# Optimization experiments

Hardware: AMD Instinct MI355X
Metric: run time of the kernel (lower is better)

## Reference

```python
import jax, jax.numpy as jnp
import numpy as np

SIG_DEPTH = 4  # matches sig_depth init arg


def _outer(a, b):
    # flattened tensor product: [B, m] x [B, n] -> [B, m*n] (row-major, matches signatory layout)
    return (a[:, :, None] * b[:, None, :]).reshape(a.shape[0], -1)


def setup_inputs() -> dict:
    key = jax.random.key(0)
    k1, k2 = jax.random.split(key)
    B, L, Cin = 64, 256, 7
    out_dim = 512
    C = Cin + 1
    sig_channels = sum(C ** k for k in range(1, SIG_DEPTH + 1))  # 4680
    inp = jax.random.normal(k1, (B, L, Cin), dtype=jnp.float32)
    W = jax.random.normal(k2, (out_dim, sig_channels), dtype=jnp.float32) * 0.02
    b = jnp.zeros((out_dim,), dtype=jnp.float32)
    return {"inp": inp, "W": W, "b": b}


def reference(inp, W, b):
    B, L, Cin = inp.shape
    # Augment: prepend time channel linspace(0, 1, L), keep original channels
    t = jnp.broadcast_to(jnp.linspace(0.0, 1.0, L, dtype=inp.dtype)[None, :, None], (B, L, 1))
    x = jnp.concatenate([t, inp], axis=-1)  # [B, L, C]
    C = Cin + 1
    d = SIG_DEPTH
    dx = jnp.transpose(x[:, 1:] - x[:, :-1], (1, 0, 2))  # [L-1, B, C] increments
    init = tuple(jnp.zeros((B, C ** (k + 1)), x.dtype) for k in range(d))  # identity signature (all zero levels)

    def step(levels, v):
        # exp(v) in the truncated tensor algebra: e_k = v^{(x)k} / k!
        e = [v]
        for k in range(1, d):
            e.append(_outer(e[-1], v) / (k + 1))
        # Chen's identity: new_k = a_k + e_k + sum_{i=1}^{k-1} a_i (x) e_{k-i}
        new = []
        for k in range(d):
            acc = levels[k] + e[k]
            for i in range(k):
                acc = acc + _outer(levels[i], e[k - 1 - i])
            new.append(acc)
        sig = jnp.concatenate(new, axis=-1)  # [B, sig_channels]
        return tuple(new), sig

    _, sigs = jax.lax.scan(step, init, dx)  # [L-1, B, sig_channels] (stream=True)
    sigs = jnp.transpose(sigs, (1, 0, 2))   # [B, L-1, sig_channels]
    return sigs @ W.T + b                   # [B, L-1, out_dim]
```

## Files before the change

### kernel.cpp

```cpp
#include <hip/hip_runtime.h>
#include <hip/hip_bf16.h>

#define BATCH 64
#define LSEQ 256
#define CIN 7
#define CC 8
#define NSIG 4680
#define KPAD 4736
#define TSTEPS 255
#define ODIM 512
#define NCHUNK 16
#define CH 16
#define NKT 74
#define BM 256
#define BN 128
#define WCVT_BLK 592

typedef __attribute__((ext_vector_type(8))) unsigned short ushort8;
typedef __attribute__((ext_vector_type(8))) __bf16 bf16x8;
typedef __attribute__((ext_vector_type(4))) float f32x4;

__device__ __forceinline__ unsigned short f2bf(float x) {
    __hip_bfloat16 h = __float2bfloat16(x);
    return *(unsigned short*)&h;
}

#define GLDS16(gp, lp)                                                      \
    __builtin_amdgcn_global_load_lds(                                       \
        (const __attribute__((address_space(1))) void*)(gp),                \
        (__attribute__((address_space(3))) void*)(lp), 16, 0, 0)

__global__ __launch_bounds__(512) void prep_kernel(const float* __restrict__ inp,
                                                   float* __restrict__ ckpt,
                                                   const float* __restrict__ W,
                                                   unsigned short* __restrict__ Wb,
                                                   int nb) {
    __shared__ float sDx[TSTEPS * CC];
    const int bx  = blockIdx.x;
    const int tid = threadIdx.x;

    if (bx < 4 * nb) {
        const int b = bx >> 2, q = bx & 3;
        const float* ip = inp + (size_t)b * LSEQ * CIN;
        for (int i = tid; i < TSTEPS * CC; i += 512) {
            int t = i >> 3, c = i & 7;
            sDx[i] = (c == 0) ? (1.0f / 255.0f)
                              : ip[(t + 1) * CIN + (c - 1)] - ip[t * CIN + (c - 1)];
        }
        __syncthreads();

        const int o  = q * 128 + (tid >> 2);
        const int e2 = tid & 3;
        const int i1 = o >> 6, i2 = (o >> 3) & 7, i3 = o & 7;
        float a1 = 0.0f, a2 = 0.0f, a3 = 0.0f, a4a = 0.0f, a4b = 0.0f;

        for (int t = 0; t < 240; ++t) {
            const float* v = &sDx[t * CC];
            const float va = v[i1], vb = v[i2], vc = v[i3];
            const float vA = v[e2], vB = v[e2 + 4];
            const float e3s = va * vb * vc * (1.0f / 6.0f);
            const float T4 = e3s * 0.25f + a1 * vb * vc * (1.0f / 6.0f)
                           + a2 * vc * 0.5f + a3;
            a4a += vA * T4;
            a4b += vB * T4;
            a3 += e3s + (a1 * vb * 0.5f + a2) * vc;
            a2 += vb * (0.5f * va + a1);
            a1 += va;

            if (((t + 1) & 15) == 0) {
                const int c = ((t + 1) >> 4) - 1;
                float* cp = ckpt + ((size_t)b * 15 + c) * NSIG;
                cp[584 + o * 8 + e2]     = a4a;
                cp[584 + o * 8 + e2 + 4] = a4b;
                if (e2 == 0) {
                    cp[72 + o] = a3;
                    if ((o & 7) == 0)  cp[8 + (o >> 3)] = a2;
                    if ((o & 63) == 0) cp[i1] = a1;
                }
            }
        }
    } else {
        const int vid = (bx - 4 * nb) * 512 + tid;
        if (vid < ODIM * (KPAD / 8)) {
            const int n = vid / (KPAD / 8);
            const int g = vid - n * (KPAD / 8);
            ushort8 pk;
            if (g < NSIG / 8) {
                const float* wp = W + (size_t)n * NSIG + g * 8;
                float4 f0 = *(const float4*)wp;
                float4 f1 = *(const float4*)(wp + 4);
                pk[0] = f2bf(f0.x); pk[1] = f2bf(f0.y);
                pk[2] = f2bf(f0.z); pk[3] = f2bf(f0.w);
                pk[4] = f2bf(f1.x); pk[5] = f2bf(f1.y);
                pk[6] = f2bf(f1.z); pk[7] = f2bf(f1.w);
            } else {
#pragma unroll
                for (int e = 0; e < 8; ++e) pk[e] = 0;
            }
            *(ushort8*)(Wb + (size_t)n * KPAD + g * 8) = pk;
        }
    }
}

__global__ __launch_bounds__(512) void sig_write_kernel(const float* __restrict__ inp,
                                                        const float* __restrict__ ckpt,
                                                        unsigned short* __restrict__ sig) {
    __shared__ float sDx[CH * CC];

    const int chunk = blockIdx.x;
    const int b     = blockIdx.y;
    const int tid   = threadIdx.x;
    const int t0    = chunk * CH;
    const int t1    = (chunk == NCHUNK - 1) ? TSTEPS : t0 + CH;

    const float* ip = inp + (size_t)b * LSEQ * CIN;
    for (int i = tid; i < (t1 - t0) * CC; i += 512) {
        int t = t0 + (i >> 3), c = i & 7;
        sDx[i] = (c == 0) ? (1.0f / 255.0f)
                          : ip[(t + 1) * CIN + (c - 1)] - ip[t * CIN + (c - 1)];
    }
    __syncthreads();

    const int i1 = tid >> 6;
    const int i2 = (tid >> 3) & 7;
    const int i3 = tid & 7;

    float a1own, a2own, a3;
    float a4[8];
    if (chunk == 0) {
        a1own = a2own = a3 = 0.0f;
#pragma unroll
        for (int e = 0; e < 8; ++e) a4[e] = 0.0f;
    } else {
        const float* cp = ckpt + ((size_t)b * 15 + (chunk - 1)) * NSIG;
        a1own = cp[i1];
        a2own = cp[8 + (tid >> 3)];
        a3    = cp[72 + tid];
        float4 q0 = *(const float4*)&cp[584 + tid * 8];
        float4 q1 = *(const float4*)&cp[584 + tid * 8 + 4];
        a4[0] = q0.x; a4[1] = q0.y; a4[2] = q0.z; a4[3] = q0.w;
        a4[4] = q1.x; a4[5] = q1.y; a4[6] = q1.z; a4[7] = q1.w;
    }

    for (int t = t0; t < t1; ++t) {
        const float* v = &sDx[(t - t0) * CC];
        const float4 vlo = *(const float4*)&v[0];
        const float4 vhi = *(const float4*)&v[4];
        const float va = v[i1], vb = v[i2], vc = v[i3];
        const float e3s = va * vb * vc * (1.0f / 6.0f);
        const float T4 = e3s * 0.25f + a1own * vb * vc * (1.0f / 6.0f)
                       + a2own * vc * 0.5f + a3;
        a4[0] += vlo.x * T4; a4[1] += vlo.y * T4;
        a4[2] += vlo.z * T4; a4[3] += vlo.w * T4;
        a4[4] += vhi.x * T4; a4[5] += vhi.y * T4;
        a4[6] += vhi.z * T4; a4[7] += vhi.w * T4;
        a3 += e3s + (a1own * vb * 0.5f + a2own) * vc;
        a2own += vb * (0.5f * va + a1own);
        a1own += va;

        unsigned short* row = sig + ((size_t)b * TSTEPS + t) * KPAD;
        ushort8 pack;
#pragma unroll
        for (int e = 0; e < 8; ++e) pack[e] = f2bf(a4[e]);
        *(ushort8*)(row + 584 + tid * 8) = pack;
        row[72 + tid] = f2bf(a3);
        if ((tid & 63) == 0) row[i1] = f2bf(a1own);
        if ((tid & 7) == 0) row[8 + (tid >> 3)] = f2bf(a2own);
        if (tid >= 448 && tid < 504) row[4232 + tid] = 0;
    }
}

__global__ __launch_bounds__(512) void gemm_kernel(const unsigned short* __restrict__ A,
                                                   const unsigned short* __restrict__ Wb,
                                                   const float* __restrict__ bias,
                                                   float* __restrict__ out,
                                                   int Mrows) {
    __shared__ unsigned short As[3][BM * 64];
    __shared__ unsigned short Bs[3][BN * 64];

    const int tid = threadIdx.x;
    int nt, mt;
    if (gridDim.y == 64) {
        const int li = blockIdx.y * 4 + blockIdx.x;
        const int x  = li & 7;
        const int j  = li >> 3;
        mt = x * 8 + (j >> 2);
        nt = j & 3;
    } else {
        nt = blockIdx.x; mt = blockIdx.y;
    }
    const int lane = tid & 63;
    const int wv   = tid >> 6;
    const int wr   = wv >> 1;
    const int wc   = wv & 1;
    const int lr   = lane & 15;
    const int lq   = lane >> 4;
    const int sb   = lr & 7;

    const f32x4 z4 = {0.0f, 0.0f, 0.0f, 0.0f};
    f32x4 acc[4][4];
#pragma unroll
    for (int i = 0; i < 4; ++i)
#pragma unroll
        for (int j = 0; j < 4; ++j) acc[i][j] = z4;

    const int srow = tid >> 3;
    const int gcb  = (tid & 7) ^ (srow & 7);
    const int scol = gcb * 8;

    const unsigned short* aptr[4];
    const unsigned short* bptr[2];
#pragma unroll
    for (int i = 0; i < 4; ++i) {
        int gr = mt * BM + i * 64 + srow;
        if (gr >= Mrows) gr = 0;
        aptr[i] = A + (size_t)gr * KPAD + scol;
    }
#pragma unroll
    for (int i = 0; i < 2; ++i)
        bptr[i] = Wb + (size_t)(nt * BN + i * 64 + srow) * KPAD + scol;

    const int kel0 = ((lq)     ^ sb) * 8;
    const int kel1 = ((4 + lq) ^ sb) * 8;
    const int aoff = (wr * 64 + lr) * 64;
    const int boff = (wc * 64 + lr) * 64;

#define STAGE_ALL(BUF, koff)                                                \
    do {                                                                    \
        _Pragma("unroll")                                                   \
        for (int i_ = 0; i_ < 4; ++i_)                                      \
            GLDS16(aptr[i_] + (koff),                                       \
                   ((char*)As[BUF]) + i_ * 8192 + tid * 16);                \
        _Pragma("unroll")                                                   \
        for (int i_ = 0; i_ < 2; ++i_)                                      \
            GLDS16(bptr[i_] + (koff),                                       \
                   ((char*)Bs[BUF]) + i_ * 8192 + tid * 16);                \
    } while (0)

#define MFMA16(AF, BF)                                                      \
    do {                                                                    \
        _Pragma("unroll")                                                   \
        for (int im_ = 0; im_ < 4; ++im_)                                   \
            _Pragma("unroll")                                               \
            for (int jm_ = 0; jm_ < 4; ++jm_)                               \
                acc[im_][jm_] = __builtin_amdgcn_mfma_f32_16x16x32_bf16(    \
                    AF[im_], BF[jm_], acc[im_][jm_], 0, 0, 0);              \
    } while (0)

#define LDF(DST, SRC, BASE, KEL)                                            \
    do {                                                                    \
        _Pragma("unroll")                                                   \
        for (int l_ = 0; l_ < 4; ++l_)                                      \
            DST[l_] = *(const bf16x8*)&SRC[(BASE) + l_ * 1024 + (KEL)];     \
    } while (0)

    bf16x8 afP[4], bfP[4], afN[4], bfN[4];

    STAGE_ALL(0, 0);
    STAGE_ALL(1, 64);
    asm volatile("s_waitcnt vmcnt(6)" ::: "memory");
    __builtin_amdgcn_sched_barrier(0);
    __builtin_amdgcn_s_barrier();
    __builtin_amdgcn_sched_barrier(0);
    LDF(afP, (&As[0][0]), aoff, kel0);
    LDF(bfP, (&Bs[0][0]), boff, kel0);
    __builtin_amdgcn_sched_barrier(0);

    int koff = 128;

#define TILE_FULL(CUR, NXT, NN)                                             \
    {                                                                       \
        LDF(afN, (&As[CUR][0]), aoff, kel1);                                \
        LDF(bfN, (&Bs[CUR][0]), boff, kel1);                                \
        STAGE_ALL(NN, koff);                                                \
        koff += 64;                                                         \
        __builtin_amdgcn_sched_barrier(0);                                  \
        asm volatile("s_waitcnt lgkmcnt(8)" ::: "memory");                  \
        __builtin_amdgcn_sched_barrier(0);                                  \
        __builtin_amdgcn_s_setprio(1);                                      \
        MFMA16(afP, bfP);                                                   \
        __builtin_amdgcn_s_setprio(0);                                      \
        __builtin_amdgcn_sched_barrier(0);                                  \
        asm volatile("s_waitcnt lgkmcnt(0)" ::: "memory");                  \
        __builtin_amdgcn_sched_barrier(0);                                  \
        asm volatile("s_waitcnt vmcnt(6)" ::: "memory");                    \
        __builtin_amdgcn_sched_barrier(0);                                  \
        __builtin_amdgcn_s_barrier();                                       \
        __builtin_amdgcn_sched_barrier(0);                                  \
        LDF(afP, (&As[NXT][0]), aoff, kel0);                                \
        LDF(bfP, (&Bs[NXT][0]), boff, kel0);                                \
        __builtin_amdgcn_sched_barrier(0);                                  \
        __builtin_amdgcn_s_setprio(1);                                      \
        MFMA16(afN, bfN);                                                   \
        __builtin_amdgcn_s_setprio(0);                                      \
        __builtin_amdgcn_sched_barrier(0);                                  \
    }

    for (int tb = 0; tb < 24; ++tb) {
        TILE_FULL(0, 1, 2);
        TILE_FULL(1, 2, 0);
        TILE_FULL(2, 0, 1);
    }

    {
        LDF(afN, (&As[0][0]), aoff, kel1);
        LDF(bfN, (&Bs[0][0]), boff, kel1);
        __builtin_amdgcn_sched_barrier(0);
        asm volatile("s_waitcnt lgkmcnt(8)" ::: "memory");
        __builtin_amdgcn_sched_barrier(0);
        __builtin_amdgcn_s_setprio(1);
        MFMA16(afP, bfP);
        __builtin_amdgcn_s_setprio(0);
        __builtin_amdgcn_sched_barrier(0);
        asm volatile("s_waitcnt lgkmcnt(0)" ::: "memory");
        __builtin_amdgcn_sched_barrier(0);
        asm volatile("s_waitcnt vmcnt(0)" ::: "memory");
        __builtin_amdgcn_sched_barrier(0);
        __builtin_amdgcn_s_barrier();
        __builtin_amdgcn_sched_barrier(0);
        LDF(afP, (&As[1][0]), aoff, kel0);
        LDF(bfP, (&Bs[1][0]), boff, kel0);
        __builtin_amdgcn_sched_barrier(0);
        __builtin_amdgcn_s_setprio(1);
        MFMA16(afN, bfN);
        __builtin_amdgcn_s_setprio(0);
        __builtin_amdgcn_sched_barrier(0);
    }
    {
        LDF(afN, (&As[1][0]), aoff, kel1);
        LDF(bfN, (&Bs[1][0]), boff, kel1);
        __builtin_amdgcn_sched_barrier(0);
        asm volatile("s_waitcnt lgkmcnt(8)" ::: "memory");
        __builtin_amdgcn_sched_barrier(0);
        __builtin_amdgcn_s_setprio(1);
        MFMA16(afP, bfP);
        __builtin_amdgcn_s_setprio(0);
        __builtin_amdgcn_sched_barrier(0);
        asm volatile("s_waitcnt lgkmcnt(0)" ::: "memory");
        __builtin_amdgcn_sched_barrier(0);
        __builtin_amdgcn_s_setprio(1);
        MFMA16(afN, bfN);
        __builtin_amdgcn_s_setprio(0);
        __builtin_amdgcn_sched_barrier(0);
    }

    float bn[4];
#pragma unroll
    for (int j = 0; j < 4; ++j)
        bn[j] = bias[nt * BN + wc * 64 + j * 16 + lr];

#pragma unroll
    for (int i = 0; i < 4; ++i) {
        const int mbase = mt * BM + wr * 64 + i * 16 + lq * 4;
#pragma unroll
        for (int r = 0; r < 4; ++r) {
            const int m = mbase + r;
            if (m < Mrows) {
#pragma unroll
                for (int j = 0; j < 4; ++j) {
                    const int n = nt * BN + wc * 64 + j * 16 + lr;
                    out[(size_t)m * ODIM + n] = acc[i][j][r] + bn[j];
                }
            }
        }
    }
#undef STAGE_ALL
#undef MFMA16
#undef LDF
#undef TILE_FULL
}

extern "C" void kernel_launch(void* const* d_in, const int* in_sizes, int n_in,
                              void* d_out, int out_size, void* d_ws, size_t ws_size,
                              hipStream_t stream) {
    const float* inp  = (const float*)d_in[0];
    const float* W    = (const float*)d_in[1];
    const float* bias = (const float*)d_in[2];
    float* out = (float*)d_out;

    const size_t wbBytes = (size_t)ODIM * KPAD * sizeof(unsigned short);
    const size_t sigPB   = (size_t)TSTEPS * KPAD * sizeof(unsigned short);
    const size_t ckptPB  = (size_t)15 * NSIG * sizeof(float);
    const size_t perB    = sigPB + ckptPB;

    int nbMax = (int)((ws_size - wbBytes) / perB);
    if (nbMax > BATCH) nbMax = BATCH;
    if (nbMax < 1) nbMax = 1;

    unsigned short* sig  = (unsigned short*)d_ws;
    float*          ckpt = (float*)((char*)d_ws + (size_t)nbMax * sigPB);
    unsigned short* Wb   = (unsigned short*)((char*)d_ws + (ws_size - wbBytes));

    for (int b0 = 0; b0 < BATCH; b0 += nbMax) {
        const int nb = (b0 + nbMax <= BATCH) ? nbMax : (BATCH - b0);
        const int Mrows = nb * TSTEPS;
        const float* ipb = inp + (size_t)b0 * LSEQ * CIN;
        prep_kernel<<<4 * nb + WCVT_BLK, 512, 0, stream>>>(ipb, ckpt, W, Wb, nb);
        sig_write_kernel<<<dim3(NCHUNK, nb), 512, 0, stream>>>(ipb, ckpt, sig);
        gemm_kernel<<<dim3(ODIM / BN, (Mrows + BM - 1) / BM), 512, 0, stream>>>(
            sig, Wb, bias, out + (size_t)b0 * TSTEPS * ODIM, Mrows);
    }
}
```

Baseline: 147.7 us.

## Load GEMM B operand directly from global into registers, bypassing LDS

The weight (B) tile is no longer staged through shared memory. Each wave loads its own B fragments straight from global memory into registers with double-buffered register sets, and only the A tile still goes through LDS. This frees LDS capacity and LDS read bandwidth, and removes the B share of the barrier-gated staging. The cost is more global traffic, since B rows are no longer shared between the two wave rows, plus higher register pressure and exposed global-load latency that the vmcnt waits now have to cover.

```diff
diff --git a/kernel.cpp b/kernel.cpp
--- a/kernel.cpp
+++ b/kernel.cpp
@@ -176,7 +176,6 @@
                                                    float* __restrict__ out,
                                                    int Mrows) {
     __shared__ unsigned short As[3][BM * 64];
-    __shared__ unsigned short Bs[3][BN * 64];
 
     const int tid = threadIdx.x;
     int nt, mt;
@@ -209,32 +208,41 @@
     const int scol = gcb * 8;
 
     const unsigned short* aptr[4];
-    const unsigned short* bptr[2];
 #pragma unroll
     for (int i = 0; i < 4; ++i) {
         int gr = mt * BM + i * 64 + srow;
         if (gr >= Mrows) gr = 0;
         aptr[i] = A + (size_t)gr * KPAD + scol;
     }
-#pragma unroll
-    for (int i = 0; i < 2; ++i)
-        bptr[i] = Wb + (size_t)(nt * BN + i * 64 + srow) * KPAD + scol;
+
+    const unsigned short* bRow0 = Wb + (size_t)(nt * BN + wc * 64 +  0 + lr) * KPAD + lq * 8;
+    const unsigned short* bRow1 = Wb + (size_t)(nt * BN + wc * 64 + 16 + lr) * KPAD + lq * 8;
+    const unsigned short* bRow2 = Wb + (size_t)(nt * BN + wc * 64 + 32 + lr) * KPAD + lq * 8;
+    const unsigned short* bRow3 = Wb + (size_t)(nt * BN + wc * 64 + 48 + lr) * KPAD + lq * 8;
 
     const int kel0 = ((lq)     ^ sb) * 8;
     const int kel1 = ((4 + lq) ^ sb) * 8;
     const int aoff = (wr * 64 + lr) * 64;
-    const int boff = (wc * 64 + lr) * 64;
-
-#define STAGE_ALL(BUF, koff)                                                \
+
+#define STAGE_A(BUF, koff)                                                  \
     do {                                                                    \
         _Pragma("unroll")                                                   \
         for (int i_ = 0; i_ < 4; ++i_)                                      \
             GLDS16(aptr[i_] + (koff),                                       \
                    ((char*)As[BUF]) + i_ * 8192 + tid * 16);                \
-        _Pragma("unroll")                                                   \
-        for (int i_ = 0; i_ < 2; ++i_)                                      \
-            GLDS16(bptr[i_] + (koff),                                       \
-                   ((char*)Bs[BUF]) + i_ * 8192 + tid * 16);                \
+    } while (0)
+
+#define LOADB(BP, BNv)                                                      \
+    do {                                                                    \
+        BP[0]  = *(const bf16x8*)(bRow0);                                   \
+        BNv[0] = *(const bf16x8*)(bRow0 + 32);                              \
+        BP[1]  = *(const bf16x8*)(bRow1);                                   \
+        BNv[1] = *(const bf16x8*)(bRow1 + 32);                              \
+        BP[2]  = *(const bf16x8*)(bRow2);                                   \
+        BNv[2] = *(const bf16x8*)(bRow2 + 32);                              \
+        BP[3]  = *(const bf16x8*)(bRow3);                                   \
+        BNv[3] = *(const bf16x8*)(bRow3 + 32);                              \
+        bRow0 += 64; bRow1 += 64; bRow2 += 64; bRow3 += 64;                 \
     } while (0)
 
 #define MFMA16(AF, BF)                                                      \
@@ -247,99 +255,95 @@
                     AF[im_], BF[jm_], acc[im_][jm_], 0, 0, 0);              \
     } while (0)
 
-#define LDF(DST, SRC, BASE, KEL)                                            \
+#define LDF(DST, BUF, KEL)                                                  \
     do {                                                                    \
         _Pragma("unroll")                                                   \
         for (int l_ = 0; l_ < 4; ++l_)                                      \
-            DST[l_] = *(const bf16x8*)&SRC[(BASE) + l_ * 1024 + (KEL)];     \
+            DST[l_] = *(const bf16x8*)&As[BUF][aoff + l_ * 1024 + (KEL)];   \
     } while (0)
 
-    bf16x8 afP[4], bfP[4], afN[4], bfN[4];
-
-    STAGE_ALL(0, 0);
-    STAGE_ALL(1, 64);
-    asm volatile("s_waitcnt vmcnt(6)" ::: "memory");
+    bf16x8 afP[4], afN[4];
+    bf16x8 b0P[4], b0N[4], b1P[4], b1N[4];
+
+    STAGE_A(0, 0);
+    STAGE_A(1, 64);
+    LOADB(b0P, b0N);
+    asm volatile("s_waitcnt vmcnt(12)" ::: "memory");
     __builtin_amdgcn_sched_barrier(0);
     __builtin_amdgcn_s_barrier();
     __builtin_amdgcn_sched_barrier(0);
-    LDF(afP, (&As[0][0]), aoff, kel0);
-    LDF(bfP, (&Bs[0][0]), boff, kel0);
+    LDF(afP, 0, kel0);
     __builtin_amdgcn_sched_barrier(0);
 
     int koff = 128;
 
-#define TILE_FULL(CUR, NXT, NN)                                             \
+#define TILE_FULL(CUR, NXT, NN, BPc, BNc, BPn, BNn)                         \
     {                                                                       \
-        LDF(afN, (&As[CUR][0]), aoff, kel1);                                \
-        LDF(bfN, (&Bs[CUR][0]), boff, kel1);                                \
-        STAGE_ALL(NN, koff);                                                \
+        LDF(afN, CUR, kel1);                                                \
+        STAGE_A(NN, koff);                                                  \
         koff += 64;                                                         \
-        __builtin_amdgcn_sched_barrier(0);                                  \
-        asm volatile("s_waitcnt lgkmcnt(8)" ::: "memory");                  \
+        LOADB(BPn, BNn);                                                    \
+        __builtin_amdgcn_sched_barrier(0);                                  \
+        asm volatile("s_waitcnt vmcnt(12) lgkmcnt(4)" ::: "memory");        \
         __builtin_amdgcn_sched_barrier(0);                                  \
         __builtin_amdgcn_s_setprio(1);                                      \
-        MFMA16(afP, bfP);                                                   \
+        MFMA16(afP, BPc);                                                   \
         __builtin_amdgcn_s_setprio(0);                                      \
         __builtin_amdgcn_sched_barrier(0);                                  \
         asm volatile("s_waitcnt lgkmcnt(0)" ::: "memory");                  \
         __builtin_amdgcn_sched_barrier(0);                                  \
-        asm volatile("s_waitcnt vmcnt(6)" ::: "memory");                    \
-        __builtin_amdgcn_sched_barrier(0);                                  \
         __builtin_amdgcn_s_barrier();                                       \
         __builtin_amdgcn_sched_barrier(0);                                  \
-        LDF(afP, (&As[NXT][0]), aoff, kel0);                                \
-        LDF(bfP, (&Bs[NXT][0]), boff, kel0);                                \
+        LDF(afP, NXT, kel0);                                                \
         __builtin_amdgcn_sched_barrier(0);                                  \
         __builtin_amdgcn_s_setprio(1);                                      \
-        MFMA16(afN, bfN);                                                   \
+        MFMA16(afN, BNc);                                                   \
         __builtin_amdgcn_s_setprio(0);                                      \
         __builtin_amdgcn_sched_barrier(0);                                  \
     }
 
-    for (int tb = 0; tb < 24; ++tb) {
-        TILE_FULL(0, 1, 2);
-        TILE_FULL(1, 2, 0);
-        TILE_FULL(2, 0, 1);
+    for (int tb = 0; tb < 12; ++tb) {
+        TILE_FULL(0, 1, 2, b0P, b0N, b1P, b1N);
+        TILE_FULL(1, 2, 0, b1P, b1N, b0P, b0N);
+        TILE_FULL(2, 0, 1, b0P, b0N, b1P, b1N);
+        TILE_FULL(0, 1, 2, b1P, b1N, b0P, b0N);
+        TILE_FULL(1, 2, 0, b0P, b0N, b1P, b1N);
+        TILE_FULL(2, 0, 1, b1P, b1N, b0P, b0N);
     }
 
     {
-        LDF(afN, (&As[0][0]), aoff, kel1);
-        LDF(bfN, (&Bs[0][0]), boff, kel1);
-        __builtin_amdgcn_sched_barrier(0);
-        asm volatile("s_waitcnt lgkmcnt(8)" ::: "memory");
+        LDF(afN, 0, kel1);
+        __builtin_amdgcn_sched_barrier(0);
+        asm volatile("s_waitcnt vmcnt(0) lgkmcnt(4)" ::: "memory");
         __builtin_amdgcn_sched_barrier(0);
         __builtin_amdgcn_s_setprio(1);
-        MFMA16(afP, bfP);
+        MFMA16(afP, b0P);
         __builtin_amdgcn_s_setprio(0);
         __builtin_amdgcn_sched_barrier(0);
         asm volatile("s_waitcnt lgkmcnt(0)" ::: "memory");
         __builtin_amdgcn_sched_barrier(0);
-        asm volatile("s_waitcnt vmcnt(0)" ::: "memory");
-        __builtin_amdgcn_sched_barrier(0);
         __builtin_amdgcn_s_barrier();
         __builtin_amdgcn_sched_barrier(0);
-        LDF(afP, (&As[1][0]), aoff, kel0);
-        LDF(bfP, (&Bs[1][0]), boff, kel0);
+        LDF(afP, 1, kel0);
         __builtin_amdgcn_sched_barrier(0);
         __builtin_amdgcn_s_setprio(1);
-        MFMA16(afN, bfN);
+        MFMA16(afN, b0N);
         __builtin_amdgcn_s_setprio(0);
         __builtin_amdgcn_sched_barrier(0);
     }
     {
-        LDF(afN, (&As[1][0]), aoff, kel1);
-        LDF(bfN, (&Bs[1][0]), boff, kel1);
-        __builtin_amdgcn_sched_barrier(0);
-        asm volatile("s_waitcnt lgkmcnt(8)" ::: "memory");
+        LDF(afN, 1, kel1);
+        __builtin_amdgcn_sched_barrier(0);
+        asm volatile("s_waitcnt lgkmcnt(4)" ::: "memory");
         __builtin_amdgcn_sched_barrier(0);
         __builtin_amdgcn_s_setprio(1);
-        MFMA16(afP, bfP);
+        MFMA16(afP, b1P);
         __builtin_amdgcn_s_setprio(0);
         __builtin_amdgcn_sched_barrier(0);
         asm volatile("s_waitcnt lgkmcnt(0)" ::: "memory");
         __builtin_amdgcn_sched_barrier(0);
         __builtin_amdgcn_s_setprio(1);
-        MFMA16(afN, bfN);
+        MFMA16(afN, b1N);
         __builtin_amdgcn_s_setprio(0);
         __builtin_amdgcn_sched_barrier(0);
     }
@@ -364,7 +368,8 @@
             }
         }
     }
-#undef STAGE_ALL
+#undef STAGE_A
+#undef LOADB
 #undef MFMA16
 #undef LDF
 #undef TILE_FULL
```

Result: slower. 243.1 us (+64.6%).

## Compute GEMM on per-step signature increments and prefix-sum outputs in epilogue

Applied to the files above, without the earlier changes.

Since the output is linear in the signature, the GEMM now multiplies per-step increments instead of full cumulative signatures, then does a prefix sum over time inside the GEMM epilogue. Level-4 increments are rank-1 (T4 outer v), so they are built on the fly in registers from a small fp32 T4 table and per-row v vectors rather than materialising the 4096-wide level-4 block in HBM. This removes most of the signature write traffic and the level-4 checkpoint state, at the cost of an in-kernel scan, extra conversion ALU work in the MFMA loop, and a different bf16 rounding profile (increments are rounded rather than cumulative values).

```diff
diff --git a/kernel.cpp b/kernel.cpp
--- a/kernel.cpp
+++ b/kernel.cpp
@@ -6,14 +6,15 @@
 #define CIN 7
 #define CC 8
 #define NSIG 4680
-#define KPAD 4736
 #define TSTEPS 255
 #define ODIM 512
 #define NCHUNK 16
 #define CH 16
-#define NKT 74
-#define BM 256
-#define BN 128
+#define ROWS 256
+#define DCOLS 640
+#define KPAD 4736
+#define NT123 20
+#define NTILES 84
 #define WCVT_BLK 592
 
 typedef __attribute__((ext_vector_type(8))) unsigned short ushort8;
@@ -39,8 +40,8 @@
     const int bx  = blockIdx.x;
     const int tid = threadIdx.x;
 
-    if (bx < 4 * nb) {
-        const int b = bx >> 2, q = bx & 3;
+    if (bx < nb) {
+        const int b = bx;
         const float* ip = inp + (size_t)b * LSEQ * CIN;
         for (int i = tid; i < TSTEPS * CC; i += 512) {
             int t = i >> 3, c = i & 7;
@@ -48,45 +49,33 @@
                               : ip[(t + 1) * CIN + (c - 1)] - ip[t * CIN + (c - 1)];
         }
         __syncthreads();
-
-        const int o  = q * 128 + (tid >> 2);
-        const int e2 = tid & 3;
-        const int i1 = o >> 6, i2 = (o >> 3) & 7, i3 = o & 7;
-        float a1 = 0.0f, a2 = 0.0f, a3 = 0.0f, a4a = 0.0f, a4b = 0.0f;
-
+        const int i1 = tid >> 6, i2 = (tid >> 3) & 7, i3 = tid & 7;
+        float a1 = 0.0f, a2 = 0.0f, a3 = 0.0f;
         for (int t = 0; t < 240; ++t) {
             const float* v = &sDx[t * CC];
             const float va = v[i1], vb = v[i2], vc = v[i3];
-            const float vA = v[e2], vB = v[e2 + 4];
             const float e3s = va * vb * vc * (1.0f / 6.0f);
-            const float T4 = e3s * 0.25f + a1 * vb * vc * (1.0f / 6.0f)
-                           + a2 * vc * 0.5f + a3;
-            a4a += vA * T4;
-            a4b += vB * T4;
             a3 += e3s + (a1 * vb * 0.5f + a2) * vc;
             a2 += vb * (0.5f * va + a1);
             a1 += va;
-
             if (((t + 1) & 15) == 0) {
                 const int c = ((t + 1) >> 4) - 1;
-                float* cp = ckpt + ((size_t)b * 15 + c) * NSIG;
-                cp[584 + o * 8 + e2]     = a4a;
-                cp[584 + o * 8 + e2 + 4] = a4b;
-                if (e2 == 0) {
-                    cp[72 + o] = a3;
-                    if ((o & 7) == 0)  cp[8 + (o >> 3)] = a2;
-                    if ((o & 63) == 0) cp[i1] = a1;
-                }
+                float* cp = ckpt + ((size_t)b * 15 + c) * 584;
+                if ((tid & 63) == 0) cp[i1] = a1;
+                if ((tid & 7) == 0) cp[8 + (tid >> 3)] = a2;
+                cp[72 + tid] = a3;
             }
         }
     } else {
-        const int vid = (bx - 4 * nb) * 512 + tid;
+        const int vid = (bx - nb) * 512 + tid;
         if (vid < ODIM * (KPAD / 8)) {
             const int n = vid / (KPAD / 8);
             const int g = vid - n * (KPAD / 8);
             ushort8 pk;
-            if (g < NSIG / 8) {
-                const float* wp = W + (size_t)n * NSIG + g * 8;
+            const float* wp = nullptr;
+            if (g < 73)      wp = W + (size_t)n * NSIG + g * 8;
+            else if (g >= 80) wp = W + (size_t)n * NSIG + 584 + (g - 80) * 8;
+            if (wp) {
                 float4 f0 = *(const float4*)wp;
                 float4 f1 = *(const float4*)(wp + 4);
                 pk[0] = f2bf(f0.x); pk[1] = f2bf(f0.y);
@@ -102,11 +91,12 @@
     }
 }
 
-__global__ __launch_bounds__(512) void sig_write_kernel(const float* __restrict__ inp,
-                                                        const float* __restrict__ ckpt,
-                                                        unsigned short* __restrict__ sig) {
+__global__ __launch_bounds__(512) void delta_kernel(const float* __restrict__ inp,
+                                                    const float* __restrict__ ckpt,
+                                                    unsigned short* __restrict__ sigD,
+                                                    float* __restrict__ T4g,
+                                                    float* __restrict__ vtab) {
     __shared__ float sDx[CH * CC];
-
     const int chunk = blockIdx.x;
     const int b     = blockIdx.y;
     const int tid   = threadIdx.x;
@@ -121,62 +111,55 @@
     }
     __syncthreads();
 
-    const int i1 = tid >> 6;
-    const int i2 = (tid >> 3) & 7;
-    const int i3 = tid & 7;
-
-    float a1own, a2own, a3;
-    float a4[8];
+    const int i1 = tid >> 6, i2 = (tid >> 3) & 7, i3 = tid & 7;
+    float a1, a2, a3;
     if (chunk == 0) {
-        a1own = a2own = a3 = 0.0f;
-#pragma unroll
-        for (int e = 0; e < 8; ++e) a4[e] = 0.0f;
+        a1 = a2 = a3 = 0.0f;
     } else {
-        const float* cp = ckpt + ((size_t)b * 15 + (chunk - 1)) * NSIG;
-        a1own = cp[i1];
-        a2own = cp[8 + (tid >> 3)];
-        a3    = cp[72 + tid];
-        float4 q0 = *(const float4*)&cp[584 + tid * 8];
-        float4 q1 = *(const float4*)&cp[584 + tid * 8 + 4];
-        a4[0] = q0.x; a4[1] = q0.y; a4[2] = q0.z; a4[3] = q0.w;
-        a4[4] = q1.x; a4[5] = q1.y; a4[6] = q1.z; a4[7] = q1.w;
+        const float* cp = ckpt + ((size_t)b * 15 + (chunk - 1)) * 584;
+        a1 = cp[i1];
+        a2 = cp[8 + (tid >> 3)];
+        a3 = cp[72 + tid];
     }
 
     for (int t = t0; t < t1; ++t) {
         const float* v = &sDx[(t - t0) * CC];
-        const float4 vlo = *(const float4*)&v[0];
-        const float4 vhi = *(const float4*)&v[4];
         const float va = v[i1], vb = v[i2], vc = v[i3];
         const float e3s = va * vb * vc * (1.0f / 6.0f);
-        const float T4 = e3s * 0.25f + a1own * vb * vc * (1.0f / 6.0f)
-                       + a2own * vc * 0.5f + a3;
-        a4[0] += vlo.x * T4; a4[1] += vlo.y * T4;
-        a4[2] += vlo.z * T4; a4[3] += vlo.w * T4;
-        a4[4] += vhi.x * T4; a4[5] += vhi.y * T4;
-        a4[6] += vhi.z * T4; a4[7] += vhi.w * T4;
-        a3 += e3s + (a1own * vb * 0.5f + a2own) * vc;
-        a2own += vb * (0.5f * va + a1own);
-        a1own += va;
-
-        unsigned short* row = sig + ((size_t)b * TSTEPS + t) * KPAD;
-        ushort8 pack;
-#pragma unroll
-        for (int e = 0; e < 8; ++e) pack[e] = f2bf(a4[e]);
-        *(ushort8*)(row + 584 + tid * 8) = pack;
-        row[72 + tid] = f2bf(a3);
-        if ((tid & 63) == 0) row[i1] = f2bf(a1own);
-        if ((tid & 7) == 0) row[8 + (tid >> 3)] = f2bf(a2own);
-        if (tid >= 448 && tid < 504) row[4232 + tid] = 0;
+        const float dT4 = e3s * 0.25f + a1 * vb * vc * (1.0f / 6.0f)
+                        + a2 * vc * 0.5f + a3;
+        const float dA3 = e3s + (a1 * vb * 0.5f + a2) * vc;
+        const float dA2 = vb * (0.5f * va + a1);
+
+        const size_t rr = (size_t)b * ROWS + t;
+        T4g[rr * 512 + tid] = dT4;
+        unsigned short* row = sigD + rr * DCOLS;
+        row[72 + tid] = f2bf(dA3);
+        if ((tid & 63) == 0) row[i1] = f2bf(va);
+        if ((tid & 7) == 0) row[8 + (tid >> 3)] = f2bf(dA2);
+        if (tid >= 448 && tid < 504) row[136 + tid] = 0;
+        if (tid >= 504) vtab[rr * 8 + (tid - 504)] = v[tid - 504];
+
+        a3 += dA3; a2 += dA2; a1 += va;
+    }
+
+    if (chunk == NCHUNK - 1) {
+        const size_t rr = (size_t)b * ROWS + 255;
+        T4g[rr * 512 + tid] = 0.0f;
+        for (int c = tid; c < DCOLS; c += 512) sigD[rr * DCOLS + c] = 0;
+        if (tid < 8) vtab[rr * 8 + tid] = 0.0f;
     }
 }
 
-__global__ __launch_bounds__(512) void gemm_kernel(const unsigned short* __restrict__ A,
+__global__ __launch_bounds__(512) void gemm_kernel(const unsigned short* __restrict__ sigD,
+                                                   const float* __restrict__ T4g,
+                                                   const float* __restrict__ vtab,
                                                    const unsigned short* __restrict__ Wb,
                                                    const float* __restrict__ bias,
-                                                   float* __restrict__ out,
-                                                   int Mrows) {
-    __shared__ unsigned short As[3][BM * 64];
-    __shared__ unsigned short Bs[3][BN * 64];
+                                                   float* __restrict__ out) {
+    __shared__ unsigned short A123[3][256 * 32];
+    __shared__ unsigned short Bs[3][128 * 64];
+    __shared__ float T4s[3][256 * 8];
 
     const int tid = threadIdx.x;
     int nt, mt;
@@ -189,13 +172,14 @@
     } else {
         nt = blockIdx.x; mt = blockIdx.y;
     }
+    const int b    = mt;
     const int lane = tid & 63;
     const int wv   = tid >> 6;
     const int wr   = wv >> 1;
     const int wc   = wv & 1;
     const int lr   = lane & 15;
     const int lq   = lane >> 4;
-    const int sb   = lr & 7;
+    const int t4k  = (lr >> 2) & 1;
 
     const f32x4 z4 = {0.0f, 0.0f, 0.0f, 0.0f};
     f32x4 acc[4][4];
@@ -204,37 +188,49 @@
 #pragma unroll
         for (int j = 0; j < 4; ++j) acc[i][j] = z4;
 
-    const int srow = tid >> 3;
-    const int gcb  = (tid & 7) ^ (srow & 7);
-    const int scol = gcb * 8;
-
-    const unsigned short* aptr[4];
-    const unsigned short* bptr[2];
+    float vreg[4][8];
 #pragma unroll
     for (int i = 0; i < 4; ++i) {
-        int gr = mt * BM + i * 64 + srow;
-        if (gr >= Mrows) gr = 0;
-        aptr[i] = A + (size_t)gr * KPAD + scol;
-    }
-#pragma unroll
-    for (int i = 0; i < 2; ++i)
-        bptr[i] = Wb + (size_t)(nt * BN + i * 64 + srow) * KPAD + scol;
-
-    const int kel0 = ((lq)     ^ sb) * 8;
-    const int kel1 = ((4 + lq) ^ sb) * 8;
-    const int aoff = (wr * 64 + lr) * 64;
-    const int boff = (wc * 64 + lr) * 64;
-
-#define STAGE_ALL(BUF, koff)                                                \
+        const float* vp = vtab + ((size_t)b * ROWS + wr * 64 + i * 16 + lr) * 8;
+        float4 v0 = *(const float4*)vp;
+        float4 v1 = *(const float4*)(vp + 4);
+        vreg[i][0] = v0.x; vreg[i][1] = v0.y; vreg[i][2] = v0.z; vreg[i][3] = v0.w;
+        vreg[i][4] = v1.x; vreg[i][5] = v1.y; vreg[i][6] = v1.z; vreg[i][7] = v1.w;
+    }
+
+    const int sr123  = tid >> 2;
+    const int scol32 = (((tid & 3) ^ (sr123 & 3)) * 8);
+    const int sr64   = tid >> 3;
+    const int scol64 = (((tid & 7) ^ (sr64 & 7)) * 8);
+    const int rT4    = tid >> 1;
+    const int hT4    = (tid & 1) ^ ((rT4 >> 2) & 1);
+
+    const int kel32 = (lq ^ (lr & 3)) * 8;
+    const int kel0  = ((lq) ^ (lr & 7)) * 8;
+    const int kel1  = ((4 + lq) ^ (lr & 7)) * 8;
+
+#define STAGE(TT)                                                           \
     do {                                                                    \
-        _Pragma("unroll")                                                   \
-        for (int i_ = 0; i_ < 4; ++i_)                                      \
-            GLDS16(aptr[i_] + (koff),                                       \
-                   ((char*)As[BUF]) + i_ * 8192 + tid * 16);                \
-        _Pragma("unroll")                                                   \
-        for (int i_ = 0; i_ < 2; ++i_)                                      \
-            GLDS16(bptr[i_] + (koff),                                       \
-                   ((char*)Bs[BUF]) + i_ * 8192 + tid * 16);                \
+        const int tt_ = (TT);                                               \
+        if (tt_ < NT123) {                                                  \
+            const int bf_ = tt_ % 3;                                        \
+            _Pragma("unroll")                                               \
+            for (int i_ = 0; i_ < 2; ++i_)                                  \
+                GLDS16(sigD + ((size_t)b * ROWS + i_ * 128 + sr123) * DCOLS \
+                            + tt_ * 32 + scol32,                            \
+                       (char*)A123[bf_] + i_ * 8192 + tid * 16);            \
+            GLDS16(Wb + (size_t)(nt * 128 + sr123) * KPAD + tt_ * 32 + scol32, \
+                   (char*)Bs[bf_] + tid * 16);                              \
+        } else {                                                            \
+            const int ot_ = tt_ - NT123;                                    \
+            GLDS16(T4g + ((size_t)b * ROWS + rT4) * 512 + ot_ * 8 + hT4 * 4,\
+                   (char*)T4s[ot_ % 3] + tid * 16);                         \
+            _Pragma("unroll")                                               \
+            for (int i_ = 0; i_ < 2; ++i_)                                  \
+                GLDS16(Wb + (size_t)(nt * 128 + i_ * 64 + sr64) * KPAD      \
+                            + DCOLS + ot_ * 64 + scol64,                    \
+                       (char*)Bs[tt_ % 3] + i_ * 8192 + tid * 16);          \
+        }                                                                   \
     } while (0)
 
 #define MFMA16(AF, BF)                                                      \
@@ -247,127 +243,143 @@
                     AF[im_], BF[jm_], acc[im_][jm_], 0, 0, 0);              \
     } while (0)
 
-#define LDF(DST, SRC, BASE, KEL)                                            \
+#define LDT4(DST, BUF, KS)                                                  \
     do {                                                                    \
         _Pragma("unroll")                                                   \
         for (int l_ = 0; l_ < 4; ++l_)                                      \
-            DST[l_] = *(const bf16x8*)&SRC[(BASE) + l_ * 1024 + (KEL)];     \
+            DST[l_] = *(const float*)((const char*)T4s[BUF]                 \
+                + (wr * 64 + l_ * 16 + lr) * 32 + (((KS) ^ t4k) * 16) + lq * 4); \
     } while (0)
 
-    bf16x8 afP[4], bfP[4], afN[4], bfN[4];
-
-    STAGE_ALL(0, 0);
-    STAGE_ALL(1, 64);
-    asm volatile("s_waitcnt vmcnt(6)" ::: "memory");
+#define CONSTR(AF, T4R)                                                     \
+    do {                                                                    \
+        _Pragma("unroll")                                                   \
+        for (int l_ = 0; l_ < 4; ++l_) {                                    \
+            union { unsigned short u[8]; bf16x8 v8; } cc_;                  \
+            _Pragma("unroll")                                               \
+            for (int e_ = 0; e_ < 8; ++e_)                                  \
+                cc_.u[e_] = f2bf(T4R[l_] * vreg[l_][e_]);                   \
+            AF[l_] = cc_.v8;                                                \
+        }                                                                   \
+    } while (0)
+
+    STAGE(0);
+    STAGE(1);
+    asm volatile("s_waitcnt vmcnt(3)" ::: "memory");
     __builtin_amdgcn_sched_barrier(0);
     __builtin_amdgcn_s_barrier();
     __builtin_amdgcn_sched_barrier(0);
-    LDF(afP, (&As[0][0]), aoff, kel0);
-    LDF(bfP, (&Bs[0][0]), boff, kel0);
-    __builtin_amdgcn_sched_barrier(0);
-
-    int koff = 128;
-
-#define TILE_FULL(CUR, NXT, NN)                                             \
-    {                                                                       \
-        LDF(afN, (&As[CUR][0]), aoff, kel1);                                \
-        LDF(bfN, (&Bs[CUR][0]), boff, kel1);                                \
-        STAGE_ALL(NN, koff);                                                \
-        koff += 64;                                                         \
-        __builtin_amdgcn_sched_barrier(0);                                  \
-        asm volatile("s_waitcnt lgkmcnt(8)" ::: "memory");                  \
-        __builtin_amdgcn_sched_barrier(0);                                  \
-        __builtin_amdgcn_s_setprio(1);                                      \
-        MFMA16(afP, bfP);                                                   \
-        __builtin_amdgcn_s_setprio(0);                                      \
-        __builtin_amdgcn_sched_barrier(0);                                  \
-        asm volatile("s_waitcnt lgkmcnt(0)" ::: "memory");                  \
-        __builtin_amdgcn_sched_barrier(0);                                  \
-        asm volatile("s_waitcnt vmcnt(6)" ::: "memory");                    \
-        __builtin_amdgcn_sched_barrier(0);                                  \
-        __builtin_amdgcn_s_barrier();                                       \
-        __builtin_amdgcn_sched_barrier(0);                                  \
-        LDF(afP, (&As[NXT][0]), aoff, kel0);                                \
-        LDF(bfP, (&Bs[NXT][0]), boff, kel0);                                \
-        __builtin_amdgcn_sched_barrier(0);                                  \
-        __builtin_amdgcn_s_setprio(1);                                      \
-        MFMA16(afN, bfN);                                                   \
-        __builtin_amdgcn_s_setprio(0);                                      \
-        __builtin_amdgcn_sched_barrier(0);                                  \
-    }
-
-    for (int tb = 0; tb < 24; ++tb) {
-        TILE_FULL(0, 1, 2);
-        TILE_FULL(1, 2, 0);
-        TILE_FULL(2, 0, 1);
-    }
-
-    {
-        LDF(afN, (&As[0][0]), aoff, kel1);
-        LDF(bfN, (&Bs[0][0]), boff, kel1);
-        __builtin_amdgcn_sched_barrier(0);
-        asm volatile("s_waitcnt lgkmcnt(8)" ::: "memory");
-        __builtin_amdgcn_sched_barrier(0);
-        __builtin_amdgcn_s_setprio(1);
-        MFMA16(afP, bfP);
-        __builtin_amdgcn_s_setprio(0);
-        __builtin_amdgcn_sched_barrier(0);
-        asm volatile("s_waitcnt lgkmcnt(0)" ::: "memory");
-        __builtin_amdgcn_sched_barrier(0);
-        asm volatile("s_waitcnt vmcnt(0)" ::: "memory");
-        __builtin_amdgcn_sched_barrier(0);
-        __builtin_amdgcn_s_barrier();
-        __builtin_amdgcn_sched_barrier(0);
-        LDF(afP, (&As[1][0]), aoff, kel0);
-        LDF(bfP, (&Bs[1][0]), boff, kel0);
-        __builtin_amdgcn_sched_barrier(0);
-        __builtin_amdgcn_s_setprio(1);
-        MFMA16(afN, bfN);
-        __builtin_amdgcn_s_setprio(0);
-        __builtin_amdgcn_sched_barrier(0);
-    }
-    {
-        LDF(afN, (&As[1][0]), aoff, kel1);
-        LDF(bfN, (&Bs[1][0]), boff, kel1);
-        __builtin_amdgcn_sched_barrier(0);
-        asm volatile("s_waitcnt lgkmcnt(8)" ::: "memory");
-        __builtin_amdgcn_sched_barrier(0);
-        __builtin_amdgcn_s_setprio(1);
-        MFMA16(afP, bfP);
-        __builtin_amdgcn_s_setprio(0);
-        __builtin_amdgcn_sched_barrier(0);
-        asm volatile("s_waitcnt lgkmcnt(0)" ::: "memory");
-        __builtin_amdgcn_sched_barrier(0);
-        __builtin_amdgcn_s_setprio(1);
-        MFMA16(afN, bfN);
-        __builtin_amdgcn_s_setprio(0);
-        __builtin_amdgcn_sched_barrier(0);
-    }
-
-    float bn[4];
-#pragma unroll
-    for (int j = 0; j < 4; ++j)
-        bn[j] = bias[nt * BN + wc * 64 + j * 16 + lr];
-
-#pragma unroll
-    for (int i = 0; i < 4; ++i) {
-        const int mbase = mt * BM + wr * 64 + i * 16 + lq * 4;
-#pragma unroll
-        for (int r = 0; r < 4; ++r) {
-            const int m = mbase + r;
-            if (m < Mrows) {
-#pragma unroll
-                for (int j = 0; j < 4; ++j) {
-                    const int n = nt * BN + wc * 64 + j * 16 + lr;
-                    out[(size_t)m * ODIM + n] = acc[i][j][r] + bn[j];
-                }
+
+    for (int t = 0; t < NTILES; ++t) {
+        if (t + 2 < NTILES) STAGE(t + 2);
+
+        if (t < NT123) {
+            const int bf = t % 3;
+            bf16x8 af[4], bfv[4];
+#pragma unroll
+            for (int l = 0; l < 4; ++l)
+                af[l] = *(const bf16x8*)&A123[bf][(wr * 64 + l * 16 + lr) * 32 + kel32];
+#pragma unroll
+            for (int l = 0; l < 4; ++l)
+                bfv[l] = *(const bf16x8*)&Bs[bf][(wc * 64 + l * 16 + lr) * 32 + kel32];
+            __builtin_amdgcn_sched_barrier(0);
+            asm volatile("s_waitcnt lgkmcnt(0)" ::: "memory");
+            __builtin_amdgcn_sched_barrier(0);
+            __builtin_amdgcn_s_setprio(1);
+            MFMA16(af, bfv);
+            __builtin_amdgcn_s_setprio(0);
+            __builtin_amdgcn_sched_barrier(0);
+        } else {
+            const int tb = (t - NT123) % 3, bb = t % 3;
+            float t4P[4], t4N[4];
+            bf16x8 bfP[4], bfN[4];
+            LDT4(t4P, tb, 0);
+#pragma unroll
+            for (int l = 0; l < 4; ++l)
+                bfP[l] = *(const bf16x8*)&Bs[bb][(wc * 64 + l * 16 + lr) * 64 + kel0];
+            LDT4(t4N, tb, 1);
+#pragma unroll
+            for (int l = 0; l < 4; ++l)
+                bfN[l] = *(const bf16x8*)&Bs[bb][(wc * 64 + l * 16 + lr) * 64 + kel1];
+            __builtin_amdgcn_sched_barrier(0);
+            asm volatile("s_waitcnt lgkmcnt(8)" ::: "memory");
+            __builtin_amdgcn_sched_barrier(0);
+            bf16x8 afP[4];
+            CONSTR(afP, t4P);
+            __builtin_amdgcn_s_setprio(1);
+            MFMA16(afP, bfP);
+            __builtin_amdgcn_s_setprio(0);
+            __builtin_amdgcn_sched_barrier(0);
+            asm volatile("s_waitcnt lgkmcnt(0)" ::: "memory");
+            __builtin_amdgcn_sched_barrier(0);
+            bf16x8 afN[4];
+            CONSTR(afN, t4N);
+            __builtin_amdgcn_s_setprio(1);
+            MFMA16(afN, bfN);
+            __builtin_amdgcn_s_setprio(0);
+            __builtin_amdgcn_sched_barrier(0);
+        }
+
+        if (t + 2 < NTILES) {
+            asm volatile("s_waitcnt vmcnt(3)" ::: "memory");
+            __builtin_amdgcn_sched_barrier(0);
+            __builtin_amdgcn_s_barrier();
+            __builtin_amdgcn_sched_barrier(0);
+        } else if (t + 1 < NTILES) {
+            asm volatile("s_waitcnt vmcnt(0)" ::: "memory");
+            __builtin_amdgcn_sched_barrier(0);
+            __builtin_amdgcn_s_barrier();
+            __builtin_amdgcn_sched_barrier(0);
+        }
+    }
+
+    float (*P)[32] = (float (*)[32])(&A123[0][0]);
+    float* S = (float*)(&T4s[0][0]);
+    const int colP = wc * 16 + lr;
+
+    for (int jj = 0; jj < 4; ++jj) {
+        __syncthreads();
+#pragma unroll
+        for (int i = 0; i < 4; ++i)
+#pragma unroll
+            for (int r = 0; r < 4; ++r)
+                P[wr * 64 + i * 16 + lq * 4 + r][colP] = acc[i][jj][r];
+        __syncthreads();
+        if (tid < 256) {
+            const int c = tid & 31, s = tid >> 5;
+            float ss = 0.0f;
+            for (int k = 0; k < 32; ++k) ss += P[s * 32 + k][c];
+            S[s * 32 + c] = ss;
+        }
+        __syncthreads();
+        if (tid < 32) {
+            float run = 0.0f;
+            for (int s = 0; s < 8; ++s) {
+                float x = S[s * 32 + tid];
+                S[s * 32 + tid] = run;
+                run += x;
             }
         }
-    }
-#undef STAGE_ALL
+        __syncthreads();
+        if (tid < 256) {
+            const int c = tid & 31, s = tid >> 5;
+            float run = S[s * 32 + c];
+            for (int k = 0; k < 32; ++k) {
+                run += P[s * 32 + k][c];
+                P[s * 32 + k][c] = run;
+            }
+        }
+        __syncthreads();
+        for (int e = tid; e < 255 * 32; e += 512) {
+            const int t = e >> 5, c = e & 31;
+            const int n = nt * 128 + (c >> 4) * 64 + jj * 16 + (c & 15);
+            out[((size_t)(b * 255 + t)) * ODIM + n] = P[t][c] + bias[n];
+        }
+    }
+#undef STAGE
 #undef MFMA16
-#undef LDF
-#undef TILE_FULL
+#undef LDT4
+#undef CONSTR
 }
 
 extern "C" void kernel_launch(void* const* d_in, const int* in_sizes, int n_in,
@@ -379,25 +391,28 @@
     float* out = (float*)d_out;
 
     const size_t wbBytes = (size_t)ODIM * KPAD * sizeof(unsigned short);
-    const size_t sigPB   = (size_t)TSTEPS * KPAD * sizeof(unsigned short);
-    const size_t ckptPB  = (size_t)15 * NSIG * sizeof(float);
-    const size_t perB    = sigPB + ckptPB;
+    const size_t sigPB   = (size_t)ROWS * DCOLS * sizeof(unsigned short);
+    const size_t t4PB    = (size_t)ROWS * 512 * sizeof(float);
+    const size_t vPB     = (size_t)ROWS * 8 * sizeof(float);
+    const size_t ckptPB  = (size_t)15 * 584 * sizeof(float);
+    const size_t perB    = sigPB + t4PB + vPB + ckptPB;
 
     int nbMax = (int)((ws_size - wbBytes) / perB);
     if (nbMax > BATCH) nbMax = BATCH;
     if (nbMax < 1) nbMax = 1;
 
-    unsigned short* sig  = (unsigned short*)d_ws;
-    float*          ckpt = (float*)((char*)d_ws + (size_t)nbMax * sigPB);
+    unsigned short* sigD = (unsigned short*)d_ws;
+    float*          T4g  = (float*)((char*)d_ws + (size_t)nbMax * sigPB);
+    float*          vtab = (float*)((char*)T4g + (size_t)nbMax * t4PB);
+    float*          ckpt = (float*)((char*)vtab + (size_t)nbMax * vPB);
     unsigned short* Wb   = (unsigned short*)((char*)d_ws + (ws_size - wbBytes));
 
     for (int b0 = 0; b0 < BATCH; b0 += nbMax) {
         const int nb = (b0 + nbMax <= BATCH) ? nbMax : (BATCH - b0);
-        const int Mrows = nb * TSTEPS;
         const float* ipb = inp + (size_t)b0 * LSEQ * CIN;
-        prep_kernel<<<4 * nb + WCVT_BLK, 512, 0, stream>>>(ipb, ckpt, W, Wb, nb);
-        sig_write_kernel<<<dim3(NCHUNK, nb), 512, 0, stream>>>(ipb, ckpt, sig);
-        gemm_kernel<<<dim3(ODIM / BN, (Mrows + BM - 1) / BM), 512, 0, stream>>>(
-            sig, Wb, bias, out + (size_t)b0 * TSTEPS * ODIM, Mrows);
+        prep_kernel<<<nb + WCVT_BLK, 512, 0, stream>>>(ipb, ckpt, W, Wb, nb);
+        delta_kernel<<<dim3(NCHUNK, nb), 512, 0, stream>>>(ipb, ckpt, sigD, T4g, vtab);
+        gemm_kernel<<<dim3(4, nb), 512, 0, stream>>>(
+            sigD, T4g, vtab, Wb, bias, out + (size_t)b0 * TSTEPS * ODIM);
     }
 }
```

Result: slower. 186.9 us (+26.5%).
